# Optimization experiments

Measured on AMD Instinct MI355X. Metric: run time of the kernel, lower is better.

Reference implementation:

```python
import jax, jax.numpy as jnp
import numpy as np
from jax import lax

# hyperparams (match init_kwargs)
DIM = 192      # dim
QK = 192       # qk_dim
HEADS = 8
GS = 128       # group_size
MLP = 384      # mlp_dim
M = 64         # num_tokens
B, H, W = 4, 128, 128


def setup_inputs() -> dict:
    key = jax.random.key(0)
    ks = jax.random.split(key, 12)
    def n(k, sh, sc=0.02):
        return jax.random.normal(k, sh, dtype=jnp.float32) * sc
    return {
        "x": n(ks[0], (B, DIM, H, W), 1.0),
        "ln_g": jnp.ones((DIM,), jnp.float32),
        "ln_b": jnp.zeros((DIM,), jnp.float32),
        "Wq": n(ks[1], (DIM, QK)),
        "Wk": n(ks[2], (DIM, QK)),
        "Wv": n(ks[3], (DIM, DIM)),
        "Wproj": n(ks[4], (DIM, DIM)),
        "Wkg": n(ks[5], (DIM, QK)),      # IRCA global-key projection of means
        "Wvg": n(ks[6], (DIM, DIM)),     # IRCA global-value projection of means
        "means": n(ks[7], (M, DIM), 1.0),  # token dictionary buffer
        "Wconv": n(ks[8], (DIM, DIM)),   # 1x1 conv (no bias) as matrix
        "mlp_ln_g": jnp.ones((DIM,), jnp.float32),
        "mlp_ln_b": jnp.zeros((DIM,), jnp.float32),
        "W_fc1": n(ks[9], (DIM, MLP)),
        "dw": n(ks[10], (MLP, 1, 3, 3)),  # depthwise 3x3 in ConvFFN
        "W_fc2": n(ks[11], (MLP, DIM)),
    }


def _ln(x, g, b, eps=1e-5):
    mu = x.mean(-1, keepdims=True)
    var = ((x - mu) ** 2).mean(-1, keepdims=True)
    return (x - mu) * lax.rsqrt(var + eps) * g + b


def _attn(q, k, v):
    scale = q.shape[-1] ** -0.5
    s = jnp.einsum('...qd,...kd->...qk', q, k) * scale
    p = jax.nn.softmax(s, axis=-1)
    return jnp.einsum('...qk,...kd->...qd', p, v)


def reference(x, ln_g, ln_b, Wq, Wk, Wv, Wproj, Wkg, Wvg, means,
              Wconv, mlp_ln_g, mlp_ln_b, W_fc1, dw, W_fc2):
    b, C, h, w = x.shape
    N = h * w
    xt = x.reshape(b, C, N).transpose(0, 2, 1)          # b n c
    residual = xt
    xn = _ln(xt, ln_g, ln_b)

    # IRCA: per-head global K/V from the token dictionary (means)
    kg = (means @ Wkg).reshape(M, HEADS, QK // HEADS).transpose(1, 0, 2)   # h m dq
    vg = (means @ Wvg).reshape(M, HEADS, C // HEADS).transpose(1, 0, 2)    # h m dv

    # cluster assignment (no-grad): cosine sim to means, argsort by cluster id
    xs = lax.stop_gradient(xn)
    ms = lax.stop_gradient(means)
    xs_n = xs / (jnp.linalg.norm(xs, axis=-1, keepdims=True) + 1e-12)
    ms_n = ms / (jnp.linalg.norm(ms, axis=-1, keepdims=True) + 1e-12)
    belong = jnp.argmax(xs_n @ ms_n.T, axis=-1)          # b n
    idx = jnp.argsort(belong, axis=-1)                   # b n, cluster-sorted order

    # IASA: project, gather into cluster-sorted order
    q = jnp.take_along_axis(xn @ Wq, idx[:, :, None], axis=1)
    k = jnp.take_along_axis(xn @ Wk, idx[:, :, None], axis=1)
    v = jnp.take_along_axis(xn @ Wv, idx[:, :, None], axis=1)

    gs = min(N, GS)
    ng = (N + gs - 1) // gs
    pad_n = ng * gs - N
    pq = jnp.concatenate([q, q[:, N - pad_n:N][:, ::-1]], axis=1)
    pq = pq.reshape(b, ng, gs, HEADS, -1).transpose(0, 1, 3, 2, 4)  # b ng h gs dq

    def windows(t):
        tr = jnp.concatenate([t, t[:, N - pad_n - gs:N][:, ::-1]], axis=1)  # len ng*gs+gs
        t1 = tr[:, :ng * gs].reshape(b, ng, gs, -1)
        t2 = tr[:, gs:].reshape(b, ng, gs, -1)
        tw = jnp.concatenate([t1, t2], axis=2)           # b ng 2gs c
        return tw.reshape(b, ng, 2 * gs, HEADS, -1).transpose(0, 1, 3, 2, 4)

    kw, vw = windows(k), windows(v)
    out1 = _attn(pq, kw, vw)                             # local overlapping windows
    out2 = _attn(pq, kg[None, None], vg[None, None])     # global dictionary attention
    out = (out1 + out2).transpose(0, 1, 3, 2, 4).reshape(b, ng * gs, C)[:, :N]

    # scatter back to original token order (idx is a permutation)
    inv = jnp.argsort(idx, axis=-1)
    out = jnp.take_along_axis(out, inv[:, :, None], axis=1)
    out = (out @ Wproj) @ Wconv                           # proj + 1x1 conv (no bias)
    xt = residual + out

    # PreNorm ConvFFN: LN -> fc1 -> depthwise 3x3 -> GELU -> fc2, residual
    h1 = _ln(xt, mlp_ln_g, mlp_ln_b) @ W_fc1              # b n mlp
    himg = h1.transpose(0, 2, 1).reshape(b, MLP, h, w)
    dwc = lax.conv_general_dilated(himg, dw, (1, 1), 'SAME',
                                   feature_group_count=MLP,
                                   dimension_numbers=('NCHW', 'OIHW', 'NCHW'))
    h2 = jax.nn.gelu(dwc.reshape(b, MLP, N).transpose(0, 2, 1))
    xt = xt + h2 @ W_fc2
    return xt.transpose(0, 2, 1).reshape(b, C, h, w)
```

## Files before the change

kernel.cpp:

```cpp
#include <hip/hip_runtime.h>

using u16 = unsigned short;
using u32 = unsigned int;
typedef __attribute__((ext_vector_type(8))) short short8;
typedef __attribute__((ext_vector_type(4))) short s16x4;
typedef __attribute__((ext_vector_type(4))) float f32x4;
typedef __attribute__((ext_vector_type(2))) float f32x2;
typedef __attribute__((ext_vector_type(4))) u16 u16x4;
typedef __attribute__((ext_vector_type(4))) u32 u32x4;

constexpr int CB   = 4;
constexpr int CC   = 192;
constexpr int CN   = 16384;
constexpr int BN   = CB * CN;
constexpr int CMLP = 384;

__device__ __forceinline__ float b2f(u16 u){ return __uint_as_float(((u32)u) << 16); }
__device__ __forceinline__ u16 f2b(float f){
  u32 u = __float_as_uint(f);
  u32 r = (u + 0x7FFFu + ((u >> 16) & 1u)) >> 16;
  return (u16)r;
}
__device__ __forceinline__ short8 ld8(const u16* p) {
  s16x4 a = *(const s16x4*)p;
  s16x4 b = *(const s16x4*)(p + 4);
  short8 r;
  r[0]=a[0]; r[1]=a[1]; r[2]=a[2]; r[3]=a[3];
  r[4]=b[0]; r[5]=b[1]; r[6]=b[2]; r[7]=b[3];
  return r;
}
__device__ __forceinline__ u32 pk_bf16(float lo, float hi) {
  u32 r;
  asm("v_cvt_pk_bf16_f32 %0, %1, %2" : "=v"(r) : "v"(lo), "v"(hi));
  return r;
}
__device__ __forceinline__ float exp2_fast(float x) {
  float r;
  asm("v_exp_f32 %0, %1" : "=v"(r) : "v"(x));
  return r;
}
__device__ __forceinline__ void gl_lds16(const u16* g, u16* l) {
  __builtin_amdgcn_global_load_lds(
      (const __attribute__((address_space(1))) void*)(const void*)g,
      (__attribute__((address_space(3))) void*)(void*)l, 16, 0, 0);
}

__global__ __launch_bounds__(256) void lnqkv_k(const float* __restrict__ src,
    const float* __restrict__ gg, const float* __restrict__ bb,
    const u16* __restrict__ msnT, const u16* __restrict__ WqkvT,
    int* __restrict__ belong, u16* __restrict__ qkv)
{
  __shared__ float t[64 * 193];
  __shared__ float sg[192], sb[192];
  __shared__ float smu[64], srs[64];
  const int tid = threadIdx.x;
  const int blk = blockIdx.x;
  const int b = blk >> 8;
  const int n0 = (blk & 255) * 64;
  if (tid < 192) { sg[tid] = gg[tid]; sb[tid] = bb[tid]; }
  const size_t sbase = ((size_t)b * CC) * CN + n0;
  #pragma unroll
  for (int it = 0; it < 48; ++it) {
    int c = it * 4 + (tid >> 6);
    int tok = tid & 63;
    t[tok * 193 + c] = src[sbase + (size_t)c * CN + tok];
  }
  __syncthreads();
  {
    int tok = tid >> 2, sub = tid & 3;
    float s = 0.f, sq = 0.f;
    #pragma unroll
    for (int i = 0; i < 48; ++i) {
      float v = t[tok * 193 + sub * 48 + i];
      s += v; sq += v * v;
    }
    s  += __shfl_xor(s, 1);  s  += __shfl_xor(s, 2);
    sq += __shfl_xor(sq, 1); sq += __shfl_xor(sq, 2);
    float mu = s * (1.f / 192.f);
    float var = fmaxf(sq * (1.f / 192.f) - mu * mu, 0.f);
    float rs = rsqrtf(var + 1e-5f);
    if (sub == 0) { smu[tok] = mu; srs[tok] = rs; }
  }
  __syncthreads();

  const int wv = tid >> 6, lane = tid & 63;
  const int l15 = lane & 15, g4 = lane >> 4, q8 = g4 * 8;
  const int tok = wv * 16 + l15;
  const float mu = smu[tok], rs = srs[tok];
  short8 afm[6];
  #pragma unroll
  for (int ks = 0; ks < 6; ++ks) {
    u32x4 qq;
    #pragma unroll
    for (int j = 0; j < 4; ++j) {
      int c = ks * 32 + q8 + 2 * j;
      float v0 = (t[tok * 193 + c]     - mu) * rs * sg[c]     + sb[c];
      float v1 = (t[tok * 193 + c + 1] - mu) * rs * sg[c + 1] + sb[c + 1];
      qq[j] = pk_bf16(v0, v1);
    }
    afm[ks] = __builtin_bit_cast(short8, qq);
  }

  {
    f32x4 sacc[4];
    #pragma unroll
    for (int ct = 0; ct < 4; ++ct) {
      sacc[ct] = 0.f;
      const u16* pM = msnT + (ct * 16 + l15) * 192 + q8;
      short8 mf[6];
      #pragma unroll
      for (int ks = 0; ks < 6; ++ks) mf[ks] = *(const short8*)(pM + ks * 32);
      #pragma unroll
      for (int ks = 0; ks < 6; ++ks)
        sacc[ct] = __builtin_amdgcn_mfma_f32_16x16x32_bf16(afm[ks], mf[ks], sacc[ct], 0, 0, 0);
    }
    #pragma unroll
    for (int r = 0; r < 4; ++r) {
      float bv = -3e38f; int bi = 1 << 30;
      #pragma unroll
      for (int ct = 0; ct < 4; ++ct) {
        float v = sacc[ct][r];
        int ci = ct * 16 + l15;
        if (v > bv || (v == bv && ci < bi)) { bv = v; bi = ci; }
      }
      #pragma unroll
      for (int d = 1; d < 16; d <<= 1) {
        float ov = __shfl_xor(bv, d);
        int   oi = __shfl_xor(bi, d);
        if (ov > bv || (ov == bv && oi < bi)) { bv = ov; bi = oi; }
      }
      if (l15 == 0) belong[b * CN + n0 + wv * 16 + g4 * 4 + r] = bi;
    }
  }

  const size_t rowb = (size_t)(b * CN + n0 + wv * 16 + g4 * 4);
  #pragma unroll 4
  for (int jc = 0; jc < 36; ++jc) {
    const u16* pW = WqkvT + (size_t)(jc * 16 + l15) * 192 + q8;
    short8 wf[6];
    #pragma unroll
    for (int ks = 0; ks < 6; ++ks) wf[ks] = *(const short8*)(pW + ks * 32);
    f32x4 acc = 0.f;
    #pragma unroll
    for (int ks = 0; ks < 6; ++ks)
      acc = __builtin_amdgcn_mfma_f32_16x16x32_bf16(afm[ks], wf[ks], acc, 0, 0, 0);
    int col = jc * 16 + l15;
    #pragma unroll
    for (int r = 0; r < 4; ++r)
      qkv[(rowb + r) * 576 + col] = f2b(acc[r]);
  }
}

__global__ __launch_bounds__(192) void prep_means_k(const float* __restrict__ means,
    const float* __restrict__ Wkg, const float* __restrict__ Wvg,
    u16* __restrict__ msnT, float* __restrict__ kg, float* __restrict__ vg)
{
  __shared__ float sv[192];
  __shared__ float red[192];
  const int m = blockIdx.x, c = threadIdx.x;
  float v = means[m * 192 + c];
  sv[c] = v; red[c] = v * v;
  __syncthreads();
  for (int s = 96; s >= 3; s >>= 1) {
    if (c < s) red[c] += red[c + s];
    __syncthreads();
  }
  if (c == 0) red[0] = 1.f / (sqrtf(red[0] + red[1] + red[2]) + 1e-12f);
  __syncthreads();
  float scale = red[0];
  msnT[m * 192 + c] = f2b(v * scale);
  float a1 = 0.f, a2 = 0.f;
  for (int cc = 0; cc < 192; ++cc) {
    float mv = sv[cc];
    a1 += mv * Wkg[cc * 192 + c];
    a2 += mv * Wvg[cc * 192 + c];
  }
  int h = c / 24, d = c % 24;
  kg[h * (64 * 24) + m * 24 + d] = a1;
  vg[h * (64 * 24) + m * 24 + d] = a2;
}

__global__ __launch_bounds__(256) void wprep_k(
    const float* __restrict__ Wp, const float* __restrict__ Wc, u16* __restrict__ WpcT,
    const float* __restrict__ Wq, const float* __restrict__ Wk, const float* __restrict__ Wv,
    u16* __restrict__ WqkvT,
    const float* __restrict__ Wfc1, u16* __restrict__ Wfc1T,
    const float* __restrict__ Wfc2, u16* __restrict__ Wfc2T)
{
  int blk = blockIdx.x;
  int tid = threadIdx.x;
  if (blk < 144) {
    int e = blk * 256 + tid;
    if (e < 192 * 192) {
      int i = e / 192, j = e % 192;
      float a = 0.f;
      for (int k = 0; k < 192; ++k) a += Wp[i * 192 + k] * Wc[k * 192 + j];
      WpcT[j * 192 + i] = f2b(a);
    }
    return;
  }
  blk -= 144;
  if (blk < 432) {
    int which = blk / 144;
    int e = (blk % 144) * 256 + tid;
    const float* W = (which == 0) ? Wq : (which == 1) ? Wk : Wv;
    if (e < 192 * 192) {
      int j = e / 192, k = e % 192;
      WqkvT[which * 192 * 192 + e] = f2b(W[k * 192 + j]);
    }
    return;
  }
  blk -= 432;
  if (blk < 288) {
    int e = blk * 256 + tid;
    if (e < 192 * 384) {
      int j = e / 192, k = e % 192;
      Wfc1T[e] = f2b(Wfc1[k * 384 + j]);
    }
    return;
  }
  blk -= 288;
  {
    int e = blk * 256 + tid;
    if (e < 384 * 192) {
      int j = e / 384, k = e % 384;
      Wfc2T[e] = f2b(Wfc2[k * 192 + j]);
    }
  }
}

__global__ __launch_bounds__(256) void resid_k(const u16* __restrict__ qkv,
    const u16* __restrict__ WpcT, const float* __restrict__ x, u16* __restrict__ xt2,
    const float* __restrict__ g2, const float* __restrict__ b2,
    const u16* __restrict__ Wfc1T, u16* __restrict__ h1)
{
  __shared__ __attribute__((aligned(16))) u16 shraw[64 * 200];
  __shared__ float smu2[64], srs2[64];
  u16* lA    = shraw;
  u16* lnb16 = shraw;
  const int tid = threadIdx.x;
  const int row0 = blockIdx.x * 64;
  const int b = row0 >> 14;
  const int wv = tid >> 6, lane = tid & 63;
  const int l15 = lane & 15, g4 = lane >> 4, q8 = g4 * 8;

  #pragma unroll
  for (int j = 0; j < 6; ++j) {
    int C = (wv * 6 + j) * 64 + lane;
    int r = C / 24;
    int c = C - r * 24;
    const u16* gp = qkv + (size_t)(row0 + r) * 576 + c * 8;
    gl_lds16(gp, lA + (wv * 6 + j) * 512);
  }
  __syncthreads();
  short8 af[4][6];
  #pragma unroll
  for (int rt = 0; rt < 4; ++rt)
    #pragma unroll
    for (int ks = 0; ks < 6; ++ks)
      af[rt][ks] = *(const short8*)(lA + (rt * 16 + l15) * 192 + ks * 32 + q8);
  __syncthreads();

  const int colw = wv * 48;
  #pragma unroll
  for (int jc = 0; jc < 3; ++jc) {
    const u16* pW = WpcT + (size_t)(colw + jc * 16 + l15) * 192 + q8;
    short8 wf[6];
    #pragma unroll
    for (int ks = 0; ks < 6; ++ks) wf[ks] = *(const short8*)(pW + ks * 32);
    f32x4 acc[4];
    #pragma unroll
    for (int rt = 0; rt < 4; ++rt) acc[rt] = 0.f;
    #pragma unroll
    for (int ks = 0; ks < 6; ++ks)
      #pragma unroll
      for (int rt = 0; rt < 4; ++rt)
        acc[rt] = __builtin_amdgcn_mfma_f32_16x16x32_bf16(wf[ks], af[rt][ks], acc[rt], 0, 0, 0);
    #pragma unroll
    for (int rt = 0; rt < 4; ++rt) {
      int n = ((row0 + rt * 16) & 16383) + l15;
      #pragma unroll
      for (int r = 0; r < 4; ++r) {
        int col = colw + jc * 16 + g4 * 4 + r;
        size_t o2 = ((size_t)(b * CC + col)) * CN + n;
        float val = x[o2] + acc[rt][r];
        u16 vb = f2b(val);
        xt2[o2] = vb;
        lnb16[(rt * 16 + l15) * 200 + col] = vb;
      }
    }
  }
  __syncthreads();

  {
    int tok = tid >> 2, sub = tid & 3;
    float s = 0.f, sq = 0.f;
    #pragma unroll
    for (int i = 0; i < 48; ++i) {
      float v = b2f(lnb16[tok * 200 + sub * 48 + i]);
      s += v; sq += v * v;
    }
    s  += __shfl_xor(s, 1);  s  += __shfl_xor(s, 2);
    sq += __shfl_xor(sq, 1); sq += __shfl_xor(sq, 2);
    float mu = s * (1.f / 192.f);
    float var = fmaxf(sq * (1.f / 192.f) - mu * mu, 0.f);
    float rs = rsqrtf(var + 1e-5f);
    if (sub == 0) { smu2[tok] = mu; srs2[tok] = rs; }
  }
  __syncthreads();
  #pragma unroll
  for (int it = 0; it < 48; ++it) {
    int e = it * 256 + tid;
    int tk = e / 192, c = e % 192;
    float v = (b2f(lnb16[tk * 200 + c]) - smu2[tk]) * srs2[tk] * g2[c] + b2[c];
    lnb16[tk * 200 + c] = f2b(v);
  }
  __syncthreads();

  short8 af2[4][6];
  #pragma unroll
  for (int rt = 0; rt < 4; ++rt)
    #pragma unroll
    for (int ks = 0; ks < 6; ++ks)
      af2[rt][ks] = *(const short8*)(lnb16 + (rt * 16 + l15) * 200 + ks * 32 + q8);
  const int colw2 = wv * 96;
  #pragma unroll
  for (int jc = 0; jc < 6; ++jc) {
    const u16* pW = Wfc1T + (size_t)(colw2 + jc * 16 + l15) * 192 + q8;
    short8 wf[6];
    #pragma unroll
    for (int ks = 0; ks < 6; ++ks) wf[ks] = *(const short8*)(pW + ks * 32);
    f32x4 acc[4];
    #pragma unroll
    for (int rt = 0; rt < 4; ++rt) acc[rt] = 0.f;
    #pragma unroll
    for (int ks = 0; ks < 6; ++ks)
      #pragma unroll
      for (int rt = 0; rt < 4; ++rt)
        acc[rt] = __builtin_amdgcn_mfma_f32_16x16x32_bf16(af2[rt][ks], wf[ks], acc[rt], 0, 0, 0);
    int col = colw2 + jc * 16 + l15;
    #pragma unroll
    for (int rt = 0; rt < 4; ++rt) {
      int row = row0 + rt * 16 + g4 * 4;
      #pragma unroll
      for (int r = 0; r < 4; ++r)
        h1[(size_t)(row + r) * CMLP + col] = f2b(acc[rt][r]);
    }
  }
}

template<int KTOT, int NCOLS>
__global__ __launch_bounds__(256) void gemmF_k(const u16* __restrict__ A,
    const u16* __restrict__ Wt, const u16* __restrict__ resid,
    float* __restrict__ o, int astride)
{
  __shared__ __attribute__((aligned(16))) u16 lA[64 * 192];
  constexpr int KC = KTOT / 192;
  constexpr int WCOLS = NCOLS / 4;
  constexpr int WCT = WCOLS / 16;
  const int tid = threadIdx.x;
  const int row0 = blockIdx.x * 64;
  const int b = row0 >> 14;
  const int wv = tid >> 6, lane = tid & 63;
  const int l15 = lane & 15, g4 = lane >> 4, q8 = g4 * 8;
  const int colw = wv * WCOLS;

  f32x4 acc[WCT * 4];
  #pragma unroll
  for (int i = 0; i < WCT * 4; ++i) acc[i] = 0.f;

  #pragma unroll
  for (int kc = 0; kc < KC; ++kc) {
    if (kc) __syncthreads();
    #pragma unroll
    for (int j = 0; j < 6; ++j) {
      int C = (wv * 6 + j) * 64 + lane;
      int r = C / 24;
      int c = C - r * 24;
      const u16* gp = A + (size_t)(row0 + r) * astride + kc * 192 + c * 8;
      gl_lds16(gp, lA + (wv * 6 + j) * 512);
    }
    __syncthreads();
    short8 af[4][6];
    #pragma unroll
    for (int rt = 0; rt < 4; ++rt)
      #pragma unroll
      for (int ks = 0; ks < 6; ++ks)
        af[rt][ks] = *(const short8*)(lA + (rt * 16 + l15) * 192 + ks * 32 + q8);

    #pragma unroll
    for (int jc = 0; jc < WCT; ++jc) {
      const u16* pW = Wt + (size_t)(colw + jc * 16 + l15) * KTOT + kc * 192 + q8;
      short8 wf[6];
      #pragma unroll
      for (int ks = 0; ks < 6; ++ks) wf[ks] = *(const short8*)(pW + ks * 32);
      #pragma unroll
      for (int ks = 0; ks < 6; ++ks)
        #pragma unroll
        for (int rt = 0; rt < 4; ++rt)
          acc[jc * 4 + rt] = __builtin_amdgcn_mfma_f32_16x16x32_bf16(wf[ks], af[rt][ks], acc[jc * 4 + rt], 0, 0, 0);
    }
  }
  #pragma unroll
  for (int jc = 0; jc < WCT; ++jc)
    #pragma unroll
    for (int tt = 0; tt < 4; ++tt) {
      int n = ((row0 + tt * 16) & 16383) + l15;
      #pragma unroll
      for (int r = 0; r < 4; ++r) {
        int outcol = colw + jc * 16 + g4 * 4 + r;
        size_t o2 = ((size_t)(b * CC + outcol)) * CN + n;
        o[o2] = b2f(resid[o2]) + acc[jc * 4 + tt][r];
      }
    }
}

__global__ __launch_bounds__(256) void hist_k(const int* __restrict__ belong, int* __restrict__ histG)
{
  __shared__ int h[64];
  int tid = threadIdx.x, blk = blockIdx.x;
  if (tid < 64) h[tid] = 0;
  __syncthreads();
  int c = belong[blk * 256 + tid];
  atomicAdd(&h[c], 1);
  __syncthreads();
  if (tid < 64) histG[blk * 64 + tid] = h[tid];
}

__global__ __launch_bounds__(64) void scan_k(const int* __restrict__ histG, int* __restrict__ chunkBase)
{
  int b = blockIdx.x, c = threadIdx.x;
  int tot = 0;
  for (int ch = 0; ch < 64; ++ch) tot += histG[(b * 64 + ch) * 64 + c];
  int inc = tot;
  for (int d = 1; d < 64; d <<= 1) {
    int v = __shfl_up(inc, d);
    if (c >= d) inc += v;
  }
  int run = inc - tot;
  for (int ch = 0; ch < 64; ++ch) {
    chunkBase[(b * 64 + ch) * 64 + c] = run;
    run += histG[(b * 64 + ch) * 64 + c];
  }
}

__global__ __launch_bounds__(256) void rank_k(const int* __restrict__ belong,
    const int* __restrict__ chunkBase, int* __restrict__ idx)
{
  __shared__ int WH[4][64];
  int tid = threadIdx.x, blk = blockIdx.x;
  int b = blk >> 6, chl = blk & 63;
  int wv = tid >> 6, lane = tid & 63;
  ((int*)WH)[tid] = 0;
  __syncthreads();
  int nl = chl * 256 + tid;
  int c = belong[blk * 256 + tid];
  int rank = 0;
  for (int m = 0; m < 64; ++m) {
    unsigned long long msk = __ballot(c == m);
    if (c == m) {
      rank = __popcll(msk & ((1ull << lane) - 1ull));
      if (rank == 0) WH[wv][m] = __popcll(msk);
    }
  }
  __syncthreads();
  int off = 0;
  #pragma unroll
  for (int w = 0; w < 3; ++w) if (w < wv) off += WH[w][c];
  int pos = chunkBase[(b * 64 + chl) * 64 + c] + off + rank;
  idx[b * CN + pos] = nl;
}

__global__ __launch_bounds__(256) void attn_k(u16* __restrict__ qkv,
    const float* __restrict__ kg, const float* __restrict__ vg,
    const int* __restrict__ idx)
{
  __shared__ __attribute__((aligned(16))) u16 sK[320 * 24];
  __shared__ __attribute__((aligned(16))) u16 sVT[25 * 332];
  __shared__ u16 sidx[256];
  const int g = blockIdx.x, h = blockIdx.y, b = blockIdx.z;
  const int tid = threadIdx.x;
  const int wave = tid >> 6, lane = tid & 63;
  const int l15 = lane & 15, g4 = lane >> 4;
  const int q8 = g4 * 8;
  const size_t base = (size_t)b * CN * 576;
  const float QSC = 0.20412414523193154f * 1.4426950408889634f;
  short8 z8 = {0,0,0,0,0,0,0,0};

  {
    int p = g * 128 + tid;
    if (p >= CN) p = 2 * CN - 1 - p;
    sidx[tid] = (u16)idx[b * CN + p];
  }
  for (int e = tid; e < 332; e += 256) sVT[24 * 332 + e] = 0x3F80;
  __syncthreads();

  #pragma unroll
  for (int it = 0; it < 8; ++it) {
    int e4 = (it * 256 + tid) * 4;
    if (e4 < 7680) {
      int r = e4 / 24, c = e4 % 24;
      if (r < 256) {
        int p = sidx[r];
        *(u16x4*)(sK + r * 24 + c) =
          *(const u16x4*)(qkv + base + (size_t)p * 576 + 192 + h * 24 + c);
      } else {
        const float* kp = kg + h * 1536 + (r - 256) * 24 + c;
        u16x4 o;
        o[0] = f2b(kp[0]); o[1] = f2b(kp[1]); o[2] = f2b(kp[2]); o[3] = f2b(kp[3]);
        *(u16x4*)(sK + r * 24 + c) = o;
      }
    }
  }
  #pragma unroll
  for (int it = 0; it < 8; ++it) {
    int e4 = (it * 256 + tid) * 4;
    if (e4 < 7680) {
      int kk = e4 / 24, c = e4 % 24;
      if (kk < 256) {
        int p = sidx[kk];
        u16x4 v = *(const u16x4*)(qkv + base + (size_t)p * 576 + 384 + h * 24 + c);
        sVT[(c + 0) * 332 + kk] = v[0];
        sVT[(c + 1) * 332 + kk] = v[1];
        sVT[(c + 2) * 332 + kk] = v[2];
        sVT[(c + 3) * 332 + kk] = v[3];
      } else {
        const float* vp = vg + h * 1536 + (kk - 256) * 24 + c;
        sVT[(c + 0) * 332 + kk] = f2b(vp[0]);
        sVT[(c + 1) * 332 + kk] = f2b(vp[1]);
        sVT[(c + 2) * 332 + kk] = f2b(vp[2]);
        sVT[(c + 3) * 332 + kk] = f2b(vp[3]);
      }
    }
  }

  short8 qf[2];
  #pragma unroll
  for (int rt = 0; rt < 2; ++rt) {
    int qrow = sidx[wave * 32 + rt * 16 + l15];
    if (g4 < 3) {
      short8 raw = ld8(qkv + base + (size_t)qrow * 576 + h * 24 + q8);
      u32x4 qq;
      #pragma unroll
      for (int j = 0; j < 4; ++j) {
        float lo = b2f((u16)raw[2 * j]) * QSC;
        float hi = b2f((u16)raw[2 * j + 1]) * QSC;
        qq[j] = pk_bf16(lo, hi);
      }
      qf[rt] = __builtin_bit_cast(short8, qq);
    } else {
      qf[rt] = z8;
    }
  }
  __syncthreads();

  f32x4 O1[2][2], O2[2][2];
  #pragma unroll
  for (int rt = 0; rt < 2; ++rt)
    #pragma unroll
    for (int ct2 = 0; ct2 < 2; ++ct2) { O1[rt][ct2] = 0.f; O2[rt][ct2] = 0.f; }

  const int srcLo = ((lane & 16) << 1) + l15;
  const int srcHi = srcLo + 16;
  const bool hiSel = lane >= 32;
  f32x4 zz = 0.f;

  auto do_tile = [&](int ktile, f32x4 (*O)[2]) {
    short8 aK[4];
    #pragma unroll
    for (int ct = 0; ct < 4; ++ct)
      aK[ct] = (g4 < 3) ? ld8(sK + (ktile + ct * 16 + l15) * 24 + q8) : z8;
    short8 bV[2][2];
    #pragma unroll
    for (int kc = 0; kc < 2; ++kc)
      #pragma unroll
      for (int ct2 = 0; ct2 < 2; ++ct2) {
        int vrow = ct2 * 16 + l15;
        bV[kc][ct2] = (vrow < 25) ? ld8(sVT + vrow * 332 + ktile + kc * 32 + q8) : z8;
      }
    #pragma unroll
    for (int rt = 0; rt < 2; ++rt) {
      f32x4 p[4];
      __builtin_amdgcn_s_setprio(1);
      #pragma unroll
      for (int ct = 0; ct < 4; ++ct)
        p[ct] = __builtin_amdgcn_mfma_f32_16x16x32_bf16(aK[ct], qf[rt], zz, 0, 0, 0);
      __builtin_amdgcn_s_setprio(0);
      #pragma unroll
      for (int ct = 0; ct < 4; ++ct)
        #pragma unroll
        for (int r = 0; r < 4; ++r)
          p[ct][r] = exp2_fast(p[ct][r]);
      #pragma unroll
      for (int kc = 0; kc < 2; ++kc) {
        u32 wA0 = pk_bf16(p[kc * 2][0], p[kc * 2][1]);
        u32 wA1 = pk_bf16(p[kc * 2][2], p[kc * 2][3]);
        u32 wB0 = pk_bf16(p[kc * 2 + 1][0], p[kc * 2 + 1][1]);
        u32 wB1 = pk_bf16(p[kc * 2 + 1][2], p[kc * 2 + 1][3]);
        u32 a0 = (u32)__shfl((int)wA0, srcLo), a1 = (u32)__shfl((int)wA1, srcLo);
        u32 a2 = (u32)__shfl((int)wA0, srcHi), a3 = (u32)__shfl((int)wA1, srcHi);
        u32 b0 = (u32)__shfl((int)wB0, srcLo), b1 = (u32)__shfl((int)wB1, srcLo);
        u32 b2 = (u32)__shfl((int)wB0, srcHi), b3 = (u32)__shfl((int)wB1, srcHi);
        u32x4 fr;
        fr[0] = hiSel ? b0 : a0; fr[1] = hiSel ? b1 : a1;
        fr[2] = hiSel ? b2 : a2; fr[3] = hiSel ? b3 : a3;
        short8 aP = __builtin_bit_cast(short8, fr);
        __builtin_amdgcn_s_setprio(1);
        #pragma unroll
        for (int ct2 = 0; ct2 < 2; ++ct2)
          O[rt][ct2] = __builtin_amdgcn_mfma_f32_16x16x32_bf16(aP, bV[kc][ct2], O[rt][ct2], 0, 0, 0);
        __builtin_amdgcn_s_setprio(0);
      }
    }
  };

  do_tile(0,   O1);
  do_tile(64,  O1);
  do_tile(128, O1);
  do_tile(192, O1);
  do_tile(256, O2);

  const int lsrc = (lane & 48) + 8;
  #pragma unroll
  for (int rt = 0; rt < 2; ++rt) {
    #pragma unroll
    for (int r = 0; r < 4; ++r) {
      float s1 = __shfl(O1[rt][1][r], lsrc);
      float s2 = __shfl(O2[rt][1][r], lsrc);
      float i1 = 1.f / s1;
      float i2 = 1.f / s2;
      int tok = sidx[wave * 32 + rt * 16 + g4 * 4 + r];
      #pragma unroll
      for (int ct2 = 0; ct2 < 2; ++ct2) {
        int d = ct2 * 16 + l15;
        if (d < 24) {
          float v = O1[rt][ct2][r] * i1 + O2[rt][ct2][r] * i2;
          qkv[base + (size_t)tok * 576 + h * 24 + d] = f2b(v);
        }
      }
    }
  }
}

__global__ __launch_bounds__(256) void conv_k(const u16* __restrict__ h1,
    const float* __restrict__ dw, u16* __restrict__ h2g)
{
  __shared__ float t[1156 * 10];
  __shared__ float sdw[72];
  const int tile = blockIdx.x;
  const int jg = blockIdx.y;
  const int bb = blockIdx.z;
  const int y0 = (tile >> 2) * 32, x0 = (tile & 3) * 32;
  const int tid = threadIdx.x;
  if (tid < 72) sdw[tid] = dw[jg * 72 + tid];
  #pragma unroll
  for (int it = 0; it < 5; ++it) {
    int e = it * 256 + tid;
    if (e < 1156) {
      int yy = e / 34 - 1 + y0, xx = e % 34 - 1 + x0;
      float v[8];
      if (yy >= 0 && yy < 128 && xx >= 0 && xx < 128) {
        short8 raw = *(const short8*)(h1 + ((size_t)(bb * CN + yy * 128 + xx)) * CMLP + jg * 8);
        #pragma unroll
        for (int c = 0; c < 8; ++c) v[c] = b2f((u16)raw[c]);
      } else {
        #pragma unroll
        for (int c = 0; c < 8; ++c) v[c] = 0.f;
      }
      #pragma unroll
      for (int c = 0; c < 8; c += 2) {
        f32x2 p; p[0] = v[c]; p[1] = v[c + 1];
        *(f32x2*)(t + e * 10 + c) = p;
      }
    }
  }
  __syncthreads();
  float acc[4][8];
  #pragma unroll
  for (int px = 0; px < 4; ++px)
    #pragma unroll
    for (int c = 0; c < 8; ++c) acc[px][c] = 0.f;
  #pragma unroll
  for (int k = 0; k < 9; ++k) {
    const int dy = k / 3, dx = k % 3;
    float w[8];
    #pragma unroll
    for (int c = 0; c < 8; ++c) w[c] = sdw[c * 9 + k];
    #pragma unroll
    for (int px = 0; px < 4; ++px) {
      int idx2 = px * 256 + tid;
      int oy = idx2 >> 5, ox = idx2 & 31;
      const float* vp = t + ((oy + dy) * 34 + ox + dx) * 10;
      #pragma unroll
      for (int c = 0; c < 8; ++c) acc[px][c] += vp[c] * w[c];
    }
  }
  #pragma unroll
  for (int px = 0; px < 4; ++px) {
    int idx2 = px * 256 + tid;
    int oy = idx2 >> 5, ox = idx2 & 31;
    short8 o;
    #pragma unroll
    for (int c = 0; c < 8; ++c) {
      float a = acc[px][c];
      float u = 1.5957691216057308f * (a + 0.044715f * a * a * a);
      float gel = a / (1.f + __expf(-u));
      o[c] = (short)f2b(gel);
    }
    *(short8*)(h2g + ((size_t)(bb * CN + (y0 + oy) * 128 + x0 + ox)) * CMLP + jg * 8) = o;
  }
}

extern "C" void kernel_launch(void* const* d_in, const int* in_sizes, int n_in,
                              void* d_out, int out_size, void* d_ws, size_t ws_size,
                              hipStream_t stream)
{
  const float* x     = (const float*)d_in[0];
  const float* ln_g  = (const float*)d_in[1];
  const float* ln_b  = (const float*)d_in[2];
  const float* Wq    = (const float*)d_in[3];
  const float* Wk    = (const float*)d_in[4];
  const float* Wv    = (const float*)d_in[5];
  const float* Wproj = (const float*)d_in[6];
  const float* Wkg   = (const float*)d_in[7];
  const float* Wvg   = (const float*)d_in[8];
  const float* means = (const float*)d_in[9];
  const float* Wconv = (const float*)d_in[10];
  const float* mlp_g = (const float*)d_in[11];
  const float* mlp_b = (const float*)d_in[12];
  const float* Wfc1  = (const float*)d_in[13];
  const float* dw    = (const float*)d_in[14];
  const float* Wfc2  = (const float*)d_in[15];
  float* out = (float*)d_out;
  (void)in_sizes; (void)n_in; (void)out_size; (void)ws_size;

  char* ws = (char*)d_ws;
  size_t off = 0;
  auto alloc = [&](size_t sz) { void* p = ws + off; off += (sz + 255) & ~(size_t)255; return p; };
  u16*  qkv   = (u16*)alloc((size_t)BN * 576 * 2);
  u16*  xt2   = (u16*)alloc((size_t)BN * 192 * 2);
  u16*  h1    = (u16*)alloc((size_t)BN * 384 * 2);
  u16*  h2g   = (u16*)alloc((size_t)BN * 384 * 2);
  u16*  msnT  = (u16*)alloc(64 * 192 * 2);
  u16*  WqkvT = (u16*)alloc(576 * 192 * 2);
  u16*  WpcT  = (u16*)alloc(192 * 192 * 2);
  u16*  Wfc1T = (u16*)alloc(384 * 192 * 2);
  u16*  Wfc2T = (u16*)alloc(192 * 384 * 2);
  float* kg   = (float*)alloc(8 * 64 * 24 * 4);
  float* vg   = (float*)alloc(8 * 64 * 24 * 4);
  int*  belong = (int*)alloc(BN * 4);
  int*  idxb   = (int*)alloc(BN * 4);
  int*  histG  = (int*)alloc(256 * 64 * 4);
  int*  chunkBase = (int*)alloc(256 * 64 * 4);

  prep_means_k<<<64, 192, 0, stream>>>(means, Wkg, Wvg, msnT, kg, vg);
  wprep_k<<<1152, 256, 0, stream>>>(Wproj, Wconv, WpcT, Wq, Wk, Wv, WqkvT,
                                    Wfc1, Wfc1T, Wfc2, Wfc2T);

  lnqkv_k<<<1024, 256, 0, stream>>>(x, ln_g, ln_b, msnT, WqkvT, belong, qkv);
  hist_k<<<256, 256, 0, stream>>>(belong, histG);
  scan_k<<<4, 64, 0, stream>>>(histG, chunkBase);
  rank_k<<<256, 256, 0, stream>>>(belong, chunkBase, idxb);
  attn_k<<<dim3(128, 8, 4), 256, 0, stream>>>(qkv, kg, vg, idxb);
  resid_k<<<1024, 256, 0, stream>>>(qkv, WpcT, x, xt2, mlp_g, mlp_b, Wfc1T, h1);
  conv_k<<<dim3(16, 48, 4), 256, 0, stream>>>(h1, dw, h2g);
  gemmF_k<384, 192><<<1024, 256, 0, stream>>>(h2g, Wfc2T, xt2, out, 384);
}
```

Measured before the change: 347.4 us.

## Split fused LN+QKV kernel into LN kernel and separate tiled QKV GEMM

The fused LayerNorm+QKV kernel is split. LN now writes normalized bf16 activations to a new workspace buffer and still computes cluster assignment. A new GEMM kernel loads a 64-row tile into LDS and has each wave compute 4 row tiles against 144 output columns, so every weight fragment is reused across 64 rows instead of 16. This trades an extra round trip of the normalized activations through global memory and one more launch for better weight reuse and lower register pressure in the LN kernel.

```diff
diff --git a/kernel.cpp b/kernel.cpp
--- a/kernel.cpp
+++ b/kernel.cpp
@@ -45,10 +45,9 @@
       (__attribute__((address_space(3))) void*)(void*)l, 16, 0, 0);
 }
 
-__global__ __launch_bounds__(256) void lnqkv_k(const float* __restrict__ src,
-    const float* __restrict__ gg, const float* __restrict__ bb,
-    const u16* __restrict__ msnT, const u16* __restrict__ WqkvT,
-    int* __restrict__ belong, u16* __restrict__ qkv)
+__global__ __launch_bounds__(256) void ln_k(const float* __restrict__ src,
+    const float* __restrict__ gg, const float* __restrict__ bb, u16* __restrict__ out,
+    const u16* __restrict__ msnT, int* __restrict__ belong)
 {
   __shared__ float t[64 * 193];
   __shared__ float sg[192], sb[192];
@@ -82,26 +81,33 @@
     if (sub == 0) { smu[tok] = mu; srs[tok] = rs; }
   }
   __syncthreads();
-
-  const int wv = tid >> 6, lane = tid & 63;
-  const int l15 = lane & 15, g4 = lane >> 4, q8 = g4 * 8;
-  const int tok = wv * 16 + l15;
-  const float mu = smu[tok], rs = srs[tok];
-  short8 afm[6];
-  #pragma unroll
-  for (int ks = 0; ks < 6; ++ks) {
-    u32x4 qq;
-    #pragma unroll
-    for (int j = 0; j < 4; ++j) {
-      int c = ks * 32 + q8 + 2 * j;
-      float v0 = (t[tok * 193 + c]     - mu) * rs * sg[c]     + sb[c];
-      float v1 = (t[tok * 193 + c + 1] - mu) * rs * sg[c + 1] + sb[c + 1];
-      qq[j] = pk_bf16(v0, v1);
-    }
-    afm[ks] = __builtin_bit_cast(short8, qq);
+  const size_t obase = ((size_t)(b * CN + n0)) * CC;
+  #pragma unroll
+  for (int it = 0; it < 48; ++it) {
+    int e = it * 256 + tid;
+    int tk = e / 192, c = e % 192;
+    float v = (t[tk * 193 + c] - smu[tk]) * srs[tk] * sg[c] + sb[c];
+    out[obase + (size_t)tk * CC + c] = f2b(v);
   }
 
   {
+    const int wv = tid >> 6, lane = tid & 63;
+    const int l15 = lane & 15, g4 = lane >> 4, q8 = g4 * 8;
+    const int tok = wv * 16 + l15;
+    const float mu = smu[tok], rs = srs[tok];
+    short8 afm[6];
+    #pragma unroll
+    for (int ks = 0; ks < 6; ++ks) {
+      u32x4 qq;
+      #pragma unroll
+      for (int j = 0; j < 4; ++j) {
+        int c = ks * 32 + q8 + 2 * j;
+        float v0 = (t[tok * 193 + c]     - mu) * rs * sg[c]     + sb[c];
+        float v1 = (t[tok * 193 + c + 1] - mu) * rs * sg[c + 1] + sb[c + 1];
+        qq[j] = pk_bf16(v0, v1);
+      }
+      afm[ks] = __builtin_bit_cast(short8, qq);
+    }
     f32x4 sacc[4];
     #pragma unroll
     for (int ct = 0; ct < 4; ++ct) {
@@ -132,22 +138,55 @@
       if (l15 == 0) belong[b * CN + n0 + wv * 16 + g4 * 4 + r] = bi;
     }
   }
-
-  const size_t rowb = (size_t)(b * CN + n0 + wv * 16 + g4 * 4);
-  #pragma unroll 4
-  for (int jc = 0; jc < 36; ++jc) {
-    const u16* pW = WqkvT + (size_t)(jc * 16 + l15) * 192 + q8;
+}
+
+__global__ __launch_bounds__(256) void gemmQ_k(const u16* __restrict__ A,
+    const u16* __restrict__ Wt, u16* __restrict__ qkv)
+{
+  __shared__ __attribute__((aligned(16))) u16 lA[64 * 192];
+  const int tid = threadIdx.x;
+  const int row0 = blockIdx.x * 64;
+  const int wv = tid >> 6, lane = tid & 63;
+  const int l15 = lane & 15, g4 = lane >> 4, q8 = g4 * 8;
+  const int colw = wv * 144;
+
+  #pragma unroll
+  for (int j = 0; j < 6; ++j) {
+    int C = (wv * 6 + j) * 64 + lane;
+    int r = C / 24;
+    int c = C - r * 24;
+    gl_lds16(A + (size_t)(row0 + r) * 192 + c * 8, lA + (wv * 6 + j) * 512);
+  }
+  __syncthreads();
+  short8 af[4][6];
+  #pragma unroll
+  for (int rt = 0; rt < 4; ++rt)
+    #pragma unroll
+    for (int ks = 0; ks < 6; ++ks)
+      af[rt][ks] = *(const short8*)(lA + (rt * 16 + l15) * 192 + ks * 32 + q8);
+
+  #pragma unroll
+  for (int jc = 0; jc < 9; ++jc) {
+    const u16* pW = Wt + (size_t)(colw + jc * 16 + l15) * 192 + q8;
     short8 wf[6];
     #pragma unroll
     for (int ks = 0; ks < 6; ++ks) wf[ks] = *(const short8*)(pW + ks * 32);
-    f32x4 acc = 0.f;
+    f32x4 acc[4];
+    #pragma unroll
+    for (int rt = 0; rt < 4; ++rt) acc[rt] = 0.f;
     #pragma unroll
     for (int ks = 0; ks < 6; ++ks)
-      acc = __builtin_amdgcn_mfma_f32_16x16x32_bf16(afm[ks], wf[ks], acc, 0, 0, 0);
-    int col = jc * 16 + l15;
-    #pragma unroll
-    for (int r = 0; r < 4; ++r)
-      qkv[(rowb + r) * 576 + col] = f2b(acc[r]);
+      #pragma unroll
+      for (int rt = 0; rt < 4; ++rt)
+        acc[rt] = __builtin_amdgcn_mfma_f32_16x16x32_bf16(af[rt][ks], wf[ks], acc[rt], 0, 0, 0);
+    int col = colw + jc * 16 + l15;
+    #pragma unroll
+    for (int rt = 0; rt < 4; ++rt) {
+      int row = row0 + rt * 16 + g4 * 4;
+      #pragma unroll
+      for (int r = 0; r < 4; ++r)
+        qkv[(size_t)(row + r) * 576 + col] = f2b(acc[rt][r]);
+    }
   }
 }
 
@@ -737,6 +776,7 @@
   char* ws = (char*)d_ws;
   size_t off = 0;
   auto alloc = [&](size_t sz) { void* p = ws + off; off += (sz + 255) & ~(size_t)255; return p; };
+  u16*  xn    = (u16*)alloc((size_t)BN * 192 * 2);
   u16*  qkv   = (u16*)alloc((size_t)BN * 576 * 2);
   u16*  xt2   = (u16*)alloc((size_t)BN * 192 * 2);
   u16*  h1    = (u16*)alloc((size_t)BN * 384 * 2);
@@ -757,10 +797,11 @@
   wprep_k<<<1152, 256, 0, stream>>>(Wproj, Wconv, WpcT, Wq, Wk, Wv, WqkvT,
                                     Wfc1, Wfc1T, Wfc2, Wfc2T);
 
-  lnqkv_k<<<1024, 256, 0, stream>>>(x, ln_g, ln_b, msnT, WqkvT, belong, qkv);
+  ln_k<<<1024, 256, 0, stream>>>(x, ln_g, ln_b, xn, msnT, belong);
   hist_k<<<256, 256, 0, stream>>>(belong, histG);
   scan_k<<<4, 64, 0, stream>>>(histG, chunkBase);
   rank_k<<<256, 256, 0, stream>>>(belong, chunkBase, idxb);
+  gemmQ_k<<<1024, 256, 0, stream>>>(xn, WqkvT, qkv);
   attn_k<<<dim3(128, 8, 4), 256, 0, stream>>>(qkv, kg, vg, idxb);
   resid_k<<<1024, 256, 0, stream>>>(qkv, WpcT, x, xt2, mlp_g, mlp_b, Wfc1T, h1);
   conv_k<<<dim3(16, 48, 4), 256, 0, stream>>>(h1, dw, h2g);
```

Result: faster. 307.1 us (-11.6%).
